# Kernel tuning notes

Hardware: AMD Instinct MI355X
Metric: run time of the kernel (lower is better)

Reference implementation:

```python
import jax, jax.numpy as jnp
import numpy as np

D_MODEL, D_STATE, L = 512, 64, 1024
BATCH = 8


def setup_inputs() -> dict:
    key = jax.random.key(0)
    ks = jax.random.split(key, 8)
    dt_min, dt_max = 1e-3, 1e-1
    log_dt = jax.random.uniform(ks[0], (D_MODEL,)) * (np.log(dt_max) - np.log(dt_min)) + np.log(dt_min)
    log_A_real = jnp.log(0.5 * jnp.ones((D_MODEL, D_STATE)))
    A_imag = jnp.pi * jnp.tile(jnp.arange(D_STATE, dtype=jnp.float32), (D_MODEL, 1))
    B_real = jnp.ones((D_MODEL, D_STATE), jnp.float32)
    B_imag = jnp.zeros((D_MODEL, D_STATE), jnp.float32)
    C_real = jax.random.normal(ks[1], (D_MODEL, D_STATE))
    C_imag = jax.random.normal(ks[2], (D_MODEL, D_STATE))
    D = jax.random.normal(ks[3], (D_MODEL,))
    # 1x1 conv (Conv1d kernel_size=1) -> weight (2H, H), bias (2H,)
    conv_w = jax.random.normal(ks[4], (2 * D_MODEL, D_MODEL)) / np.sqrt(D_MODEL)
    conv_b = jnp.zeros((2 * D_MODEL,), jnp.float32)
    dec_w = jax.random.normal(ks[5], (1, D_MODEL)) / np.sqrt(D_MODEL)
    dec_b = jnp.zeros((1,), jnp.float32)
    u = jax.random.normal(ks[6], (BATCH, D_MODEL, L))
    return dict(u=u, log_dt=log_dt, log_A_real=log_A_real, A_imag=A_imag,
                B_real=B_real, B_imag=B_imag, C_real=C_real, C_imag=C_imag,
                D=D, conv_w=conv_w, conv_b=conv_b, dec_w=dec_w, dec_b=dec_b)


def _s4d_kernel(log_dt, log_A_real, A_imag, B_real, B_imag, C_real, C_imag, Lk):
    dt = jnp.exp(log_dt)                              # (H,)
    A = -jnp.exp(log_A_real) + 1j * A_imag            # (H, N) complex
    dtA = A * dt[:, None]                             # (H, N)
    A_bar = jnp.exp(dtA)
    Bc = B_real + 1j * B_imag
    B_bar = (A_bar - 1.0) / A * Bc                    # ZOH discretization
    Cc = C_real + 1j * C_imag
    t = jnp.arange(Lk)                                # (L,)
    # A_bar^t = exp(dtA * t); fuse C*B_bar weighting, reduce over state N
    A_pow = jnp.exp(dtA[:, :, None] * t)              # (H, N, L)
    K = jnp.einsum('hn,hnl->hl', Cc * B_bar, A_pow)   # (H, L) complex
    return K.real


def reference(u, log_dt, log_A_real, A_imag, B_real, B_imag, C_real, C_imag,
              D, conv_w, conv_b, dec_w, dec_b):
    H, Lk = u.shape[1], u.shape[2]
    K = _s4d_kernel(log_dt, log_A_real, A_imag, B_real, B_imag, C_real, C_imag, Lk)
    # depthwise cross-correlation (torch conv1d semantics), padding L-1, keep first L
    y = jax.lax.conv_general_dilated(
        u, K[:, None, :], window_strides=(1,), padding=[(Lk - 1, Lk - 1)],
        feature_group_count=H, dimension_numbers=('NCH', 'OIH', 'NCH'))
    y = y[:, :, :Lk]
    y = y + u * D[:, None]
    y = jax.nn.gelu(y, approximate=False)
    # 1x1 conv + GLU over channel dim
    z = jnp.einsum('oc,bcl->bol', conv_w, y) + conv_b[:, None]
    a, b = jnp.split(z, 2, axis=1)
    y = a * jax.nn.sigmoid(b)                         # (B, H, L)
    pooled = y.mean(axis=-1)                          # (B, H)
    return pooled @ dec_w.T + dec_b                   # (B, 1)
```

## Files before the change

kernel.cpp:

```cpp
#include <hip/hip_runtime.h>
#include <hip/hip_bf16.h>
#include <math.h>

typedef __attribute__((ext_vector_type(8))) short short8;
typedef __attribute__((ext_vector_type(4))) float f32x4;
typedef __attribute__((ext_vector_type(16))) float f32x16;
typedef __attribute__((ext_vector_type(4))) unsigned int uint4v;

constexpr int Hm = 512, Lm = 1024, Bm = 8;

static __device__ __forceinline__ unsigned short f2bf(float f) {
    __hip_bfloat16 h = __float2bfloat16(f);
    return *reinterpret_cast<unsigned short*>(&h);
}
static __device__ __forceinline__ float bf2f(unsigned short u) {
    return __uint_as_float((unsigned)u << 16);
}
static __device__ __forceinline__ uint2 pack4(const unsigned short* x) {
    return make_uint2((unsigned)x[0] | ((unsigned)x[1] << 16),
                      (unsigned)x[2] | ((unsigned)x[3] << 16));
}
static __device__ __forceinline__ short8 ld16u(const char* p) {
    uint2 a = *(const uint2*)p;
    uint2 b = *(const uint2*)(p + 8);
    uint4v t = { a.x, a.y, b.x, b.y };
    return __builtin_bit_cast(short8, t);
}

__global__ __launch_bounds__(256) void k_kgen(const float* __restrict__ log_dt,
                                              const float* __restrict__ log_A_real,
                                              const float* __restrict__ A_imag,
                                              const float* __restrict__ B_real,
                                              const float* __restrict__ B_imag,
                                              const float* __restrict__ C_real,
                                              const float* __restrict__ C_imag,
                                              const float* __restrict__ conv_w,
                                              unsigned int* __restrict__ Krep,
                                              unsigned short* __restrict__ Woh) {
    __shared__ __align__(16) char smem[22528];
    const int tid = threadIdx.x, lane = tid & 63, wid = tid >> 6;
    float* kl = (float*)smem + wid * 1056;
    float* Kf = (float*)(smem + 16896);
    float* pl = (float*)(smem + 20992);
    const int h = blockIdx.x;

    {
        int i = h * 1024 + tid * 4;
        float4 v = *(const float4*)&conv_w[i];
        *(uint2*)&Woh[i] = make_uint2((unsigned)f2bf(v.x) | ((unsigned)f2bf(v.y) << 16),
                                      (unsigned)f2bf(v.z) | ((unsigned)f2bf(v.w) << 16));
    }
    if (tid < 64) {
        int idx = h * 64 + tid;
        double dt = exp((double)log_dt[h]);
        double Ar = -exp((double)log_A_real[idx]);
        double Ai = (double)A_imag[idx];
        double ar = Ar * dt, ai = Ai * dt;
        double er = exp(ar);
        double rr = er * cos(ai), ri = er * sin(ai);
        double nr = rr - 1.0, ni = ri;
        double den = Ar * Ar + Ai * Ai;
        double qr = (nr * Ar + ni * Ai) / den;
        double qi = (ni * Ar - nr * Ai) / den;
        double Br = (double)B_real[idx], Bi = (double)B_imag[idx];
        double bbr = qr * Br - qi * Bi, bbi = qr * Bi + qi * Br;
        double Cr = (double)C_real[idx], Ci = (double)C_imag[idx];
        double wr = Cr * bbr - Ci * bbi, wi = Cr * bbi + Ci * bbr;
        double e64 = exp(ar * 64.0);
        double p64 = ai * 64.0;
        pl[0 * 64 + tid] = (float)rr;
        pl[1 * 64 + tid] = (float)ri;
        pl[2 * 64 + tid] = (float)wr;
        pl[3 * 64 + tid] = (float)wi;
        pl[4 * 64 + tid] = (float)(e64 * cos(p64));
        pl[5 * 64 + tid] = (float)(e64 * sin(p64));
    }
    __syncthreads();

    const float rrf = pl[0 * 64 + lane], rif = pl[1 * 64 + lane];
    float pr = pl[2 * 64 + lane], pi = pl[3 * 64 + lane];
    float br = pl[4 * 64 + lane], bi = pl[5 * 64 + lane];
    int cc = wid * 4;
    while (cc) {
        if (cc & 1) { float t_ = pr * br - pi * bi; pi = fmaf(pr, bi, pi * br); pr = t_; }
        float t2 = br * br - bi * bi; bi = 2.f * br * bi; br = t2;
        cc >>= 1;
    }
    const int jj = lane & 15, nq = lane >> 4;
    for (int q = 0; q < 16; ++q) {
        #pragma unroll
        for (int j = 0; j < 16; ++j) {
            kl[j * 66 + lane] = pr;
            float t_ = pr * rrf - pi * rif; pi = fmaf(pr, rif, pi * rrf); pr = t_;
        }
        asm volatile("s_waitcnt lgkmcnt(0)" ::: "memory");
        float s0 = 0.f, s1 = 0.f;
        #pragma unroll
        for (int n = 0; n < 16; n += 4) {
            float2 a = *(const float2*)&kl[jj * 66 + nq * 16 + n];
            float2 b2 = *(const float2*)&kl[jj * 66 + nq * 16 + n + 2];
            s0 += a.x + a.y; s1 += b2.x + b2.y;
        }
        float s = s0 + s1;
        s += __shfl_xor(s, 16);
        s += __shfl_xor(s, 32);
        if (lane < 16) Kf[wid * 256 + q * 16 + jj] = s;
        asm volatile("s_waitcnt lgkmcnt(0)" ::: "memory");
    }
    __syncthreads();
    for (int t = tid; t < 2200; t += 256) {
        int s = t / 550;
        int d = t - s * 550;
        int idx0 = 2 * d + s;
        float k0 = (idx0 < 1024) ? Kf[idx0] : 0.f;
        float k1 = (idx0 + 1 < 1024) ? Kf[idx0 + 1] : 0.f;
        Krep[(size_t)h * 2200 + t] = (unsigned)f2bf(k0) | ((unsigned)f2bf(k1) << 16);
    }
}

__global__ __launch_bounds__(256, 2) void k_tconv(const float* __restrict__ u,
                                                  const float* __restrict__ Dvec,
                                                  const unsigned int* __restrict__ Krep,
                                                  unsigned short* __restrict__ YbfH) {
    __shared__ __align__(16) char smem[36160];
    const int tid = threadIdx.x, lane = tid & 63, w = tid >> 6;
    const int h = blockIdx.x;
    const int m = lane & 31, q = lane >> 5;
    const int cg = (lane >> 3) & 3, b = lane & 7;

    {
        const uint4* src = (const uint4*)(Krep + (size_t)h * 2200);
        uint4* dst = (uint4*)smem;
        for (int o = tid; o < 550; o += 256) dst[o] = src[o];
    }
    if (tid < 8) { uint4 z = {0, 0, 0, 0}; ((uint4*)(smem + 36032))[tid] = z; }
    {
        const int b2 = tid >> 5, t32 = tid & 31;
        const float* ub = u + ((size_t)(b2 * 512 + h)) * 1024;
        #pragma unroll
        for (int g = 0; g < 8; ++g) {
            int s = t32 * 4 + g * 128;
            float4 v = *(const float4*)&ub[s];
            unsigned short t0 = f2bf(v.x), t1 = f2bf(v.y), t2 = f2bf(v.z), t3 = f2bf(v.w);
            int jc = s >> 6, e = s & 63;
            *(uint2*)(smem + 17600 + jc * 1152 + b2 * 144 + e * 2) =
                make_uint2((unsigned)t0 | ((unsigned)t1 << 16),
                           (unsigned)t2 | ((unsigned)t3 << 16));
        }
    }
    __syncthreads();

    const int icg = (cg == 0) ? w : (cg == 1) ? 7 - w : (cg == 2) ? 8 + w : 15 - w;
    const int dmax = 15 - w;

    int aU = 17600 + icg * 1152 + b * 144 + q * 16;
    const int zl = 36032 + q * 16;

    const int r = (3 - m) & 3;
    int baseH = r * 2200 + (991 - m - r + 8 * q) * 2;

    const f32x16 zacc = {};
    f32x16 acc0 = zacc, acc1 = zacc;

    short8 m2, m1, w0, w1, w2, w3;
    {
        const char* pH = smem + baseH;
        m2 = ld16u(pH +   0); m1 = ld16u(pH +  32);
        w0 = ld16u(pH +  64); w1 = ld16u(pH +  96);
        w2 = ld16u(pH + 128); w3 = ld16u(pH + 160);
    }

    for (int d = 0; d <= dmax; ++d) {
        const char* pb = smem + ((d <= icg) ? aU : zl);
        short8 b0 = *(const short8*)(pb +  0);
        short8 b1 = *(const short8*)(pb + 32);
        short8 b2 = *(const short8*)(pb + 64);
        short8 b3 = *(const short8*)(pb + 96);
        acc0 = __builtin_amdgcn_mfma_f32_32x32x16_bf16(w0, b0, acc0, 0, 0, 0);
        acc1 = __builtin_amdgcn_mfma_f32_32x32x16_bf16(m2, b0, acc1, 0, 0, 0);
        acc0 = __builtin_amdgcn_mfma_f32_32x32x16_bf16(w1, b1, acc0, 0, 0, 0);
        acc1 = __builtin_amdgcn_mfma_f32_32x32x16_bf16(m1, b1, acc1, 0, 0, 0);
        acc0 = __builtin_amdgcn_mfma_f32_32x32x16_bf16(w2, b2, acc0, 0, 0, 0);
        acc1 = __builtin_amdgcn_mfma_f32_32x32x16_bf16(w0, b2, acc1, 0, 0, 0);
        acc0 = __builtin_amdgcn_mfma_f32_32x32x16_bf16(w3, b3, acc0, 0, 0, 0);
        acc1 = __builtin_amdgcn_mfma_f32_32x32x16_bf16(w1, b3, acc1, 0, 0, 0);
        baseH -= 128; aU -= 1152;
        if (d < dmax) {
            const char* pH = smem + baseH;
            m2 = ld16u(pH +   0); m1 = ld16u(pH +  32);
            w0 = ld16u(pH +  64); w1 = ld16u(pH +  96);
            w2 = ld16u(pH + 128); w3 = ld16u(pH + 160);
        }
    }

    const float Dh = Dvec[h];
    __syncthreads();

    #pragma unroll
    for (int mf = 0; mf < 2; ++mf) {
        const f32x16 ac = mf ? acc1 : acc0;
        #pragma unroll
        for (int rq = 0; rq < 4; ++rq) {
            const int row0 = mf * 32 + 8 * rq + 4 * q;
            uint2 uv2 = *(const uint2*)(smem + 17600 + icg * 1152 + b * 144 + row0 * 2);
            unsigned short us[4] = { (unsigned short)(uv2.x & 0xffff),
                                     (unsigned short)(uv2.x >> 16),
                                     (unsigned short)(uv2.y & 0xffff),
                                     (unsigned short)(uv2.y >> 16) };
            unsigned short oh[4];
            #pragma unroll
            for (int k = 0; k < 4; ++k) {
                float y = ac[rq * 4 + k] + Dh * bf2f(us[k]);
                float g = 0.5f * y * (1.0f + erff(y * 0.70710678118654752f));
                oh[k] = f2bf(g);
            }
            *(uint2*)(smem + icg * 1088 + b * 136 + row0 * 2) = pack4(oh);
        }
    }
    __syncthreads();
    {
        const int b2 = tid >> 5, t32 = tid & 31;
        unsigned short* dst = YbfH + ((size_t)(b2 * 512 + h)) * 1024;
        #pragma unroll
        for (int g = 0; g < 8; ++g) {
            int s = t32 * 4 + g * 128;
            int jc = s >> 6, e = s & 63;
            uint2 v = *(const uint2*)(smem + jc * 1088 + b2 * 136 + e * 2);
            *(uint2*)&dst[s] = v;
        }
    }
}

__global__ __launch_bounds__(256) void k2_gemm(const unsigned short* __restrict__ WbfH,
                                               const unsigned short* __restrict__ Ybf,
                                               const float* __restrict__ conv_b,
                                               const float* __restrict__ dec_w,
                                               float* __restrict__ partial) {
    __shared__ unsigned short WTh[128][40];
    __shared__ unsigned short YT[128][44];
    __shared__ float red[4][64][20];
    const int tid = threadIdx.x, lane = tid & 63, wid = tid >> 6;
    const int b = blockIdx.z, oblk = blockIdx.y, lblk = blockIdx.x;
    const int o0 = oblk * 64, l0 = lblk * 128;
    const int fr = lane & 15, fq = lane >> 4;

    f32x4 acc[8][2] = {};

    const int srow = tid >> 1, skh = (tid & 1) * 16;
    const int grow = (srow < 64) ? (o0 + srow) : (512 + o0 + srow - 64);
    const size_t woff = (size_t)grow * 512 + skh;
    const int cp = tid & 15, lg = tid >> 4;

    for (int c0 = 0; c0 < 512; c0 += 32) {
        __syncthreads();
        uint4 wh0 = *(const uint4*)(WbfH + woff + c0);
        uint4 wh1 = *(const uint4*)(WbfH + woff + c0 + 8);
        const unsigned short* ys0 = Ybf + ((size_t)(b * 512 + c0 + 2 * cp)) * 1024 + l0 + lg * 8;
        uint4 y0 = *(const uint4*)ys0;
        uint4 y1 = *(const uint4*)(ys0 + 1024);
        *(uint4*)&WTh[srow][skh]     = wh0;
        *(uint4*)&WTh[srow][skh + 8] = wh1;
        {
            const unsigned int* a = (const unsigned int*)&y0;
            const unsigned int* c = (const unsigned int*)&y1;
            #pragma unroll
            for (int t2 = 0; t2 < 4; ++t2) {
                unsigned int lo = (a[t2] & 0xffffu) | (c[t2] << 16);
                unsigned int hi = (a[t2] >> 16) | (c[t2] & 0xffff0000u);
                *(unsigned int*)&YT[lg * 8 + 2 * t2][2 * cp] = lo;
                *(unsigned int*)&YT[lg * 8 + 2 * t2 + 1][2 * cp] = hi;
            }
        }
        __syncthreads();
        short8 b0h = ld16u((const char*)&YT[wid * 32 + fr][fq * 8]);
        short8 b1h = ld16u((const char*)&YT[wid * 32 + 16 + fr][fq * 8]);
        #pragma unroll
        for (int mf = 0; mf < 8; ++mf) {
            short8 ah = *(const short8*)&WTh[mf * 16 + fr][fq * 8];
            acc[mf][0] = __builtin_amdgcn_mfma_f32_16x16x32_bf16(ah, b0h, acc[mf][0], 0, 0, 0);
            acc[mf][1] = __builtin_amdgcn_mfma_f32_16x16x32_bf16(ah, b1h, acc[mf][1], 0, 0, 0);
        }
    }

    #pragma unroll
    for (int mf = 0; mf < 4; ++mf)
        #pragma unroll
        for (int j = 0; j < 4; ++j) {
            int ol = mf * 16 + fq * 4 + j;
            float ba = conv_b[o0 + ol];
            float bb = conv_b[512 + o0 + ol];
            float s = 0.f;
            #pragma unroll
            for (int nf = 0; nf < 2; ++nf) {
                float za = acc[mf][nf][j] + ba;
                float zb = acc[mf + 4][nf][j] + bb;
                s += za / (1.f + expf(-zb));
            }
            red[wid][ol][fr] = s;
        }
    __syncthreads();
    if (tid < 64) {
        float s = 0.f;
        #pragma unroll
        for (int w = 0; w < 4; ++w) {
            float4 r0 = *(const float4*)&red[w][tid][0];
            float4 r1 = *(const float4*)&red[w][tid][4];
            float4 r2 = *(const float4*)&red[w][tid][8];
            float4 r3 = *(const float4*)&red[w][tid][12];
            s += (r0.x + r0.y + r0.z + r0.w) + (r1.x + r1.y + r1.z + r1.w)
               + (r2.x + r2.y + r2.z + r2.w) + (r3.x + r3.y + r3.z + r3.w);
        }
        float val = s * dec_w[o0 + tid] * (1.0f / 1024.0f);
        #pragma unroll
        for (int off = 32; off; off >>= 1) val += __shfl_xor(val, off);
        if (tid == 0) partial[((b * 8) + oblk) * 8 + lblk] = val;
    }
}

__global__ void k3_final(const float* __restrict__ partial,
                         const float* __restrict__ dec_b,
                         float* __restrict__ out) {
    int b = threadIdx.x;
    if (b < Bm) {
        float s = dec_b[0];
        for (int i = 0; i < 64; ++i) s += partial[b * 64 + i];
        out[b] = s;
    }
}

extern "C" void kernel_launch(void* const* d_in, const int* in_sizes, int n_in,
                              void* d_out, int out_size, void* d_ws, size_t ws_size,
                              hipStream_t stream) {
    const float* u          = (const float*)d_in[0];
    const float* log_dt     = (const float*)d_in[1];
    const float* log_A_real = (const float*)d_in[2];
    const float* A_imag     = (const float*)d_in[3];
    const float* B_real     = (const float*)d_in[4];
    const float* B_imag     = (const float*)d_in[5];
    const float* C_real     = (const float*)d_in[6];
    const float* C_imag     = (const float*)d_in[7];
    const float* Dvec       = (const float*)d_in[8];
    const float* conv_w     = (const float*)d_in[9];
    const float* conv_b     = (const float*)d_in[10];
    const float* dec_w      = (const float*)d_in[11];
    const float* dec_b      = (const float*)d_in[12];

    char* base = (char*)d_ws;
    unsigned int* Krep   = (unsigned int*)base;
    unsigned short* YbfH = (unsigned short*)(base + 4718592);
    unsigned short* Wh   = (unsigned short*)(base + 13107200);
    float* partial       = (float*)(base + 14155776);
    float* out           = (float*)d_out;

    k_kgen<<<512, 256, 0, stream>>>(log_dt, log_A_real, A_imag, B_real, B_imag,
                                    C_real, C_imag, conv_w, Krep, Wh);
    k_tconv<<<512, 256, 0, stream>>>(u, Dvec, Krep, YbfH);
    k2_gemm<<<dim3(8, 8, 8), 256, 0, stream>>>(Wh, YbfH, conv_b, dec_w, partial);
    k3_final<<<1, 64, 0, stream>>>(partial, dec_b, out);
}
```

Measured before the change: 61.53 us.

## Fuse SSM kernel generation into the Toeplitz conv kernel via shared memory

```diff
diff --git a/kernel.cpp b/kernel.cpp
--- a/kernel.cpp
+++ b/kernel.cpp
@@ -27,22 +27,25 @@
     return __builtin_bit_cast(short8, t);
 }
 
-__global__ __launch_bounds__(256) void k_kgen(const float* __restrict__ log_dt,
-                                              const float* __restrict__ log_A_real,
-                                              const float* __restrict__ A_imag,
-                                              const float* __restrict__ B_real,
-                                              const float* __restrict__ B_imag,
-                                              const float* __restrict__ C_real,
-                                              const float* __restrict__ C_imag,
-                                              const float* __restrict__ conv_w,
-                                              unsigned int* __restrict__ Krep,
-                                              unsigned short* __restrict__ Woh) {
-    __shared__ __align__(16) char smem[22528];
-    const int tid = threadIdx.x, lane = tid & 63, wid = tid >> 6;
-    float* kl = (float*)smem + wid * 1056;
-    float* Kf = (float*)(smem + 16896);
-    float* pl = (float*)(smem + 20992);
+__global__ __launch_bounds__(256, 2) void k_tconv(const float* __restrict__ log_dt,
+                                                  const float* __restrict__ log_A_real,
+                                                  const float* __restrict__ A_imag,
+                                                  const float* __restrict__ B_real,
+                                                  const float* __restrict__ B_imag,
+                                                  const float* __restrict__ C_real,
+                                                  const float* __restrict__ C_imag,
+                                                  const float* __restrict__ conv_w,
+                                                  const float* __restrict__ u,
+                                                  const float* __restrict__ Dvec,
+                                                  unsigned short* __restrict__ Woh,
+                                                  unsigned short* __restrict__ YbfH) {
+    __shared__ __align__(16) char smem[36160];
+    const int tid = threadIdx.x, lane = tid & 63, w = tid >> 6;
     const int h = blockIdx.x;
+    const int m = lane & 31, q = lane >> 5;
+    const int cg = (lane >> 3) & 3, b = lane & 7;
+    float* Kf = (float*)(smem + 8800);
+    float* pl = (float*)(smem + 12896);
 
     {
         int i = h * 1024 + tid * 4;
@@ -77,63 +80,55 @@
     }
     __syncthreads();
 
-    const float rrf = pl[0 * 64 + lane], rif = pl[1 * 64 + lane];
-    float pr = pl[2 * 64 + lane], pi = pl[3 * 64 + lane];
-    float br = pl[4 * 64 + lane], bi = pl[5 * 64 + lane];
-    int cc = wid * 4;
-    while (cc) {
-        if (cc & 1) { float t_ = pr * br - pi * bi; pi = fmaf(pr, bi, pi * br); pr = t_; }
-        float t2 = br * br - bi * bi; bi = 2.f * br * bi; br = t2;
-        cc >>= 1;
-    }
-    const int jj = lane & 15, nq = lane >> 4;
-    for (int q = 0; q < 16; ++q) {
-        #pragma unroll
-        for (int j = 0; j < 16; ++j) {
-            kl[j * 66 + lane] = pr;
-            float t_ = pr * rrf - pi * rif; pi = fmaf(pr, rif, pi * rrf); pr = t_;
-        }
-        asm volatile("s_waitcnt lgkmcnt(0)" ::: "memory");
-        float s0 = 0.f, s1 = 0.f;
-        #pragma unroll
-        for (int n = 0; n < 16; n += 4) {
-            float2 a = *(const float2*)&kl[jj * 66 + nq * 16 + n];
-            float2 b2 = *(const float2*)&kl[jj * 66 + nq * 16 + n + 2];
-            s0 += a.x + a.y; s1 += b2.x + b2.y;
-        }
-        float s = s0 + s1;
-        s += __shfl_xor(s, 16);
-        s += __shfl_xor(s, 32);
-        if (lane < 16) Kf[wid * 256 + q * 16 + jj] = s;
-        asm volatile("s_waitcnt lgkmcnt(0)" ::: "memory");
-    }
-    __syncthreads();
-    for (int t = tid; t < 2200; t += 256) {
-        int s = t / 550;
-        int d = t - s * 550;
-        int idx0 = 2 * d + s;
-        float k0 = (idx0 < 1024) ? Kf[idx0] : 0.f;
-        float k1 = (idx0 + 1 < 1024) ? Kf[idx0 + 1] : 0.f;
-        Krep[(size_t)h * 2200 + t] = (unsigned)f2bf(k0) | ((unsigned)f2bf(k1) << 16);
-    }
-}
-
-__global__ __launch_bounds__(256, 2) void k_tconv(const float* __restrict__ u,
-                                                  const float* __restrict__ Dvec,
-                                                  const unsigned int* __restrict__ Krep,
-                                                  unsigned short* __restrict__ YbfH) {
-    __shared__ __align__(16) char smem[36160];
-    const int tid = threadIdx.x, lane = tid & 63, w = tid >> 6;
-    const int h = blockIdx.x;
-    const int m = lane & 31, q = lane >> 5;
-    const int cg = (lane >> 3) & 3, b = lane & 7;
-
-    {
-        const uint4* src = (const uint4*)(Krep + (size_t)h * 2200);
-        uint4* dst = (uint4*)smem;
-        for (int o = tid; o < 550; o += 256) dst[o] = src[o];
+    {
+        float* kl = (float*)(smem + 17600) + w * 1056;
+        const float rrf = pl[0 * 64 + lane], rif = pl[1 * 64 + lane];
+        float pr = pl[2 * 64 + lane], pi = pl[3 * 64 + lane];
+        float br = pl[4 * 64 + lane], bi = pl[5 * 64 + lane];
+        int cc = w * 4;
+        while (cc) {
+            if (cc & 1) { float t_ = pr * br - pi * bi; pi = fmaf(pr, bi, pi * br); pr = t_; }
+            float t2 = br * br - bi * bi; bi = 2.f * br * bi; br = t2;
+            cc >>= 1;
+        }
+        const int jj = lane & 15, nq = lane >> 4;
+        for (int qq = 0; qq < 16; ++qq) {
+            #pragma unroll
+            for (int j = 0; j < 16; ++j) {
+                kl[j * 66 + lane] = pr;
+                float t_ = pr * rrf - pi * rif; pi = fmaf(pr, rif, pi * rrf); pr = t_;
+            }
+            asm volatile("s_waitcnt lgkmcnt(0)" ::: "memory");
+            float s0 = 0.f, s1 = 0.f;
+            #pragma unroll
+            for (int n = 0; n < 16; n += 4) {
+                float2 a = *(const float2*)&kl[jj * 66 + nq * 16 + n];
+                float2 b2 = *(const float2*)&kl[jj * 66 + nq * 16 + n + 2];
+                s0 += a.x + a.y; s1 += b2.x + b2.y;
+            }
+            float s = s0 + s1;
+            s += __shfl_xor(s, 16);
+            s += __shfl_xor(s, 32);
+            if (lane < 16) Kf[w * 256 + qq * 16 + jj] = s;
+            asm volatile("s_waitcnt lgkmcnt(0)" ::: "memory");
+        }
+    }
+    __syncthreads();
+
+    {
+        unsigned int* Gd = (unsigned int*)smem;
+        for (int t = tid; t < 2200; t += 256) {
+            int s = t / 550;
+            int d = t - s * 550;
+            int idx0 = 2 * d + s;
+            float k0 = (idx0 < 1024) ? Kf[idx0] : 0.f;
+            float k1 = (idx0 + 1 < 1024) ? Kf[idx0 + 1] : 0.f;
+            Gd[t] = (unsigned)f2bf(k0) | ((unsigned)f2bf(k1) << 16);
+        }
     }
     if (tid < 8) { uint4 z = {0, 0, 0, 0}; ((uint4*)(smem + 36032))[tid] = z; }
+    __syncthreads();
+
     {
         const int b2 = tid >> 5, t32 = tid & 31;
         const float* ub = u + ((size_t)(b2 * 512 + h)) * 1024;
@@ -346,15 +341,13 @@
     const float* dec_b      = (const float*)d_in[12];
 
     char* base = (char*)d_ws;
-    unsigned int* Krep   = (unsigned int*)base;
-    unsigned short* YbfH = (unsigned short*)(base + 4718592);
-    unsigned short* Wh   = (unsigned short*)(base + 13107200);
-    float* partial       = (float*)(base + 14155776);
+    unsigned short* YbfH = (unsigned short*)base;
+    unsigned short* Wh   = (unsigned short*)(base + 8388608);
+    float* partial       = (float*)(base + 9437184);
     float* out           = (float*)d_out;
 
-    k_kgen<<<512, 256, 0, stream>>>(log_dt, log_A_real, A_imag, B_real, B_imag,
-                                    C_real, C_imag, conv_w, Krep, Wh);
-    k_tconv<<<512, 256, 0, stream>>>(u, Dvec, Krep, YbfH);
+    k_tconv<<<512, 256, 0, stream>>>(log_dt, log_A_real, A_imag, B_real, B_imag,
+                                     C_real, C_imag, conv_w, u, Dvec, Wh, YbfH);
     k2_gemm<<<dim3(8, 8, 8), 256, 0, stream>>>(Wh, YbfH, conv_b, dec_w, partial);
     k3_final<<<1, 64, 0, stream>>>(partial, dec_b, out);
 }
```

After: 56.61 us. 8.0% less time.
